# Optimization experiments

Measured on AMD Instinct MI355X. Metric: run time of the kernel, lower is better.

The kernel has to match this reference:

```python
import jax, jax.numpy as jnp
import numpy as np


def _freq_downsample(x, sf):
    # torch: stack(chunk(dim=2), 4) -> cat(chunk(dim=3), 4) -> mean(-1) -> repeat(1,1,sf,sf)
    # equivalent: mean over the sf x sf grid of contiguous blocks, then tile back.
    B, C, H, W = x.shape
    m = x.reshape(B, C, sf, H // sf, sf, W // sf).mean(axis=(2, 4))
    return jnp.tile(m, (1, 1, sf, sf))


def setup_inputs() -> dict:
    key = jax.random.key(0)
    k1, k2, k3 = jax.random.split(key, 3)
    shape = (4, 3, 256, 256)
    return {
        "STy": jax.random.normal(k1, shape, dtype=jnp.float32),
        "Fk_real": jax.random.normal(k2, shape, dtype=jnp.float32),
        "Fk_imag": jax.random.normal(k3, shape, dtype=jnp.float32),
        "sf": 2,
    }


def _forward(STy, Fk_real, Fk_imag, sf, num_iters=50, alpha=1e-6, gam=0.1):
    fft2 = lambda a: jnp.fft.fft2(a, axes=(-2, -1))
    ifft2 = lambda a: jnp.fft.ifft2(a, axes=(-2, -1))

    Fk = jax.lax.complex(Fk_real, Fk_imag)          # complex64 OTF
    FkC = jnp.conj(Fk)
    Fk2 = Fk_real ** 2 + Fk_imag ** 2               # |Fk|^2, real

    FSTy = fft2(STy)
    Fr = FkC * FSTy / (_freq_downsample(Fk2, sf) + alpha)
    pred = ifft2(Fr).real

    # finite-difference stencils DH = [1,-1] horizontal, DV vertical
    DH = jnp.zeros_like(pred).at[..., 0, 0].set(1.0).at[..., 0, 1].set(-1.0)
    DV = jnp.zeros_like(pred).at[..., 0, 0].set(1.0).at[..., 1, 0].set(-1.0)
    FDH, FDV = fft2(DH), fft2(DV)
    FDHC, FDVC = jnp.conj(FDH), jnp.conj(FDV)
    FD2 = jnp.abs(FDV) ** 2 + jnp.abs(FDH) ** 2 + 1e-8  # real

    # loop-invariant terms (identical math to recomputing each iteration)
    den = _freq_downsample(Fk2 / FD2, sf) + alpha
    FkFSTy = FkC * FSTy

    def body(carry, k):
        pred, x_old, t_old, U1, U2, D1, D2 = carry
        gam_k = gam * jnp.exp2(-k / num_iters)      # gam * 0.5 ** (k/num_iters)
        Fr = FkFSTy + alpha * (FDHC * fft2(U1 - D1) + FDVC * fft2(U2 - D2))
        Fr = (Fr - FkC * _freq_downsample(Fk * Fr / FD2, sf) / den) / (alpha * FD2)
        x_new = ifft2(Fr).real
        t_new = (1.0 + jnp.sqrt(1.0 + 4.0 * t_old ** 2)) / 2.0
        pred = x_new + (t_old - 1.0) / t_new * (x_new - x_old)
        DHr = ifft2(Fr * FDH).real
        DVr = ifft2(Fr * FDV).real
        NU1, NU2 = DHr + D1, DVr + D2
        NU = jnp.sqrt(NU1 ** 2 + NU2 ** 2 + 1e-8)
        A = jnp.maximum(0.0, NU - gam_k) + 1e-8
        A = A / (A + gam_k)                         # soft-threshold magnitude shrink
        U1n, U2n = A * NU1, A * NU2
        return (pred, x_new, t_new, U1n, U2n, D1 + DHr - U1n, D2 + DVr - U2n), None

    carry0 = (pred, pred, jnp.float32(1.0), pred, pred,
              jnp.zeros_like(pred), jnp.zeros_like(pred))
    ks = jnp.arange(num_iters, dtype=jnp.float32)
    (pred, *_), _ = jax.lax.scan(body, carry0, ks)
    return pred


def reference(STy, Fk_real, Fk_imag, sf):
    return _forward(STy, Fk_real, Fk_imag, sf)
```

## Files before the change

kernel.cpp:

```cpp
#include <hip/hip_runtime.h>
#include <math.h>

#define NIMG 12
#define NSZ 256
#define HWSZ 65536
#define NBLK 768

__device__ __forceinline__ size_t widx(int n, int u, int j)
{
  int tile = (j & 127) >> 1;
  int slot = (j & 1) + ((j >> 7) << 1);
  return ((((size_t)n << 6) + tile) << 10) + ((size_t)u << 2) + slot;
}

__device__ __forceinline__ void isync(unsigned* flags, int base, int sr, unsigned gen)
{
  __syncthreads();
  int t = threadIdx.x;
  if (t < 64) {
    if (t == 0) {
      __builtin_amdgcn_fence(__ATOMIC_RELEASE, "agent");
      __hip_atomic_store(&flags[base + sr], gen, __ATOMIC_RELAXED, __HIP_MEMORY_SCOPE_AGENT);
    }
    unsigned v;
    do {
      v = __hip_atomic_load(&flags[base + t], __ATOMIC_RELAXED, __HIP_MEMORY_SCOPE_AGENT);
    } while (__any(v < gen));
    __builtin_amdgcn_fence(__ATOMIC_ACQUIRE, "agent");
  }
  __syncthreads();
}

__device__ __forceinline__ void fft256g(float2* A, float2* B, const float2* tw, int lane,
                                        float dir, bool active)
{
  float2* src = A;
  float2* dst = B;
  int m = 1;
#pragma unroll
  for (int s = 0; s < 8; ++s) {
    __syncthreads();
    if (active) {
#pragma unroll
      for (int h = 0; h < 2; ++h) {
        int b = lane + (h << 6);
        int k = b & (m - 1);
        int jm = b - k;
        float2 a = src[b];
        float2 c = src[b + 128];
        float2 w = tw[jm];
        float wr = w.x, wi = dir * w.y;
        float ex = a.x - c.x, ey = a.y - c.y;
        dst[2 * jm + k]     = make_float2(a.x + c.x, a.y + c.y);
        dst[2 * jm + k + m] = make_float2(ex * wr - ey * wi, ex * wi + ey * wr);
      }
    }
    float2* t = src; src = dst; dst = t;
    m <<= 1;
  }
  __syncthreads();
}
__device__ __forceinline__ void fft256(float2* A, float2* B, const float2* tw, int lane, float dir)
{
  fft256g(A, B, tw, lane, dir, true);
}

__device__ __forceinline__ void make_tw(float2* tw, int t)
{
  float s, c;
  sincospif((float)t * (1.0f / 128.0f), &s, &c);
  tw[t] = make_float2(c, s);
}

__device__ __forceinline__ double fdval(const float2* tw, int k)
{
  return 2.0 - 2.0 * (double)tw[k].x;
}

__global__ __launch_bounds__(256, 3) void k_mega(const float* __restrict__ sty,
                                                 const float* __restrict__ fkr,
                                                 const float* __restrict__ fki,
                                                 float2* __restrict__ WG,
                                                 float2* __restrict__ WF,
                                                 float* __restrict__ Dh,
                                                 float* __restrict__ x49,
                                                 float* __restrict__ out,
                                                 float cmom, unsigned* flags)
{
  __shared__ float2 tw[256];
  __shared__ float2 bufA[6][256];
  __shared__ float2 scrB[6][256];
  __shared__ float2 fkL[4][256];
  __shared__ float2 kfL[4][256];
  __shared__ float  dnL[256];
  __shared__ float  D1L[4][256];
  __shared__ float  D2L[4][256];

  float*   aL   = (float*)scrB;
  float*   bL   = ((float*)scrB) + 5 * 256;
  double2* Ml   = (double2*)scrB;
  float*   dsAp = (float*)scrB;

  int t = threadIdx.x;
  make_tw(tw, t);
  int slot = ((blockIdx.x & 7) * 96) + (blockIdx.x >> 3);
  int n = slot >> 6;
  int sr = slot & 63;
  int fbase = n << 6;
  int r0 = sr << 2;
  int j0 = sr << 1;
  int w = t >> 6, lane = t & 63;
  const float sc = 1.0f / 65536.0f;
  size_t cb = ((((size_t)n << 6) + sr) << 10);
  unsigned gen = 0;

  {
    const float* src = sty + (size_t)n * HWSZ + (size_t)(r0 + w) * NSZ;
#pragma unroll
    for (int q = 0; q < 4; ++q) { int j = lane + (q << 6); bufA[w][j] = make_float2(src[j], 0.f); }
    fft256(bufA[w], scrB[w], tw, lane, -1.f);
#pragma unroll
    for (int q = 0; q < 4; ++q) { int j = lane + (q << 6); WG[widx(n, r0 + w, j)] = bufA[w][j]; }
#pragma unroll
    for (int c = 0; c < 4; ++c) {
      int gc = j0 + (c & 1) + ((c >> 1) << 7);
      size_t idx = (size_t)n * HWSZ + (size_t)t * NSZ + gc;
      fkL[c][t] = make_float2(fkr[idx], fki[idx]);
    }
  }
  isync(flags, fbase, sr, ++gen);

  {
#pragma unroll
    for (int q = 0; q < 4; ++q) { int u = lane + (q << 6); bufA[w][u] = WG[cb + (u << 2) + w]; }
    fft256(bufA[w], scrB[w], tw, lane, -1.f);
#pragma unroll
    for (int c = 0; c < 4; ++c) {
      float2 K = fkL[c][t];
      float2 f = bufA[c][t];
      kfL[c][t] = make_float2(K.x * f.x + K.y * f.y, K.x * f.y - K.y * f.x);
    }
    __syncthreads();
    {
      int u0 = t & 127, p = t >> 7;
      double s1 = 0.0, s2 = 0.0;
#pragma unroll
      for (int s = 0; s < 4; ++s) {
        int u = u0 + ((s & 1) << 7);
        int c = p + ((s >> 1) << 1);
        int gc = j0 + (c & 1) + ((c >> 1) << 7);
        double kr = fkL[c][u].x, ki = fkL[c][u].y;
        double k2 = kr * kr + ki * ki;
        double fd2 = fdval(tw, u) + fdval(tw, gc) + 1e-8;
        s1 += k2;
        s2 += k2 / fd2;
      }
      dnL[u0 * 2 + p] = (float)(s2 * 0.25 + 1e-6);
      dsAp[p * 128 + u0] = (float)(s1 * 0.25 + 1e-6);
    }
    __syncthreads();
#pragma unroll
    for (int c = 0; c < 4; ++c) {
      float d = dsAp[(c & 1) * 128 + (t & 127)];
      float2 kf = kfL[c][t];
      bufA[c][t] = make_float2(kf.x / d, kf.y / d);
    }
    fft256(bufA[w], scrB[w], tw, lane, +1.f);
#pragma unroll
    for (int q = 0; q < 4; ++q) { int u = lane + (q << 6); WF[cb + (u << 2) + w] = bufA[w][u]; }
  }
  isync(flags, fbase, sr, ++gen);

  for (int k = 0; k < 50; ++k) {
    float gamp = (k >= 1) ? (float)(0.1 * exp2(-(double)(k - 1) / 50.0)) : 0.f;

    {
      int gr = (r0 + w - 1) & 255;
#pragma unroll
      for (int q = 0; q < 4; ++q) { int j = lane + (q << 6); bufA[w][j] = WF[widx(n, gr, j)]; }
      fft256(bufA[w], scrB[w], tw, lane, +1.f);
    }
    {
      bool act = (w < 2);
      int e = 4 + (w & 1);
      int gr = (r0 + e - 1) & 255;
      if (act) {
#pragma unroll
        for (int q = 0; q < 4; ++q) { int j = lane + (q << 6); bufA[e][j] = WF[widx(n, gr, j)]; }
      }
      fft256g(bufA[e], scrB[e], tw, lane, +1.f, act);
    }
    {
      int jm1 = (t - 1) & 255;
      size_t hR = (((size_t)n << 6) + ((sr + 1) & 63)) << 9;
      size_t hW = (((size_t)n << 6) + sr) << 9;
      const float* DhP = Dh + (size_t)((k + 1) & 1) * (NBLK * 512);
      float* DhW = Dh + (size_t)(k & 1) * (NBLK * 512);
      for (int e = 1; e <= 5; ++e) {
        int gr = (r0 + e - 1) & 255;
        float xc = bufA[e][t].x * sc;
        if (k == 49 && e <= 4) x49[(size_t)n * HWSZ + (size_t)gr * NSZ + t] = xc;
        float a, b;
        if (k == 0) {
          a = xc; b = xc;
          if (e <= 4) { D1L[e - 1][t] = 0.f; D2L[e - 1][t] = 0.f; }
        } else {
          float dhr = xc - bufA[e][jm1].x * sc;
          float dvr = xc - bufA[e - 1][t].x * sc;
          float d1, d2;
          if (e <= 4) { d1 = D1L[e - 1][t]; d2 = D2L[e - 1][t]; }
          else        { d1 = DhP[hR + t];   d2 = DhP[hR + 256 + t]; }
          float nu1 = dhr + d1, nu2 = dvr + d2;
          float nu = sqrtf(nu1 * nu1 + nu2 * nu2 + 1e-8f);
          float A = fmaxf(0.f, nu - gamp) + 1e-8f;
          A = A / (A + gamp);
          float u1 = A * nu1, u2 = A * nu2;
          float d1v = d1 + dhr - u1;
          float d2v = d2 + dvr - u2;
          if (e <= 4) { D1L[e - 1][t] = d1v; D2L[e - 1][t] = d2v; }
          if (e == 1) { DhW[hW + t] = d1v; DhW[hW + 256 + t] = d2v; }
          a = u1 - d1v; b = u2 - d2v;
        }
        aL[(e - 1) * 256 + t] = a;
        bL[(e - 1) * 256 + t] = b;
      }
    }
    __syncthreads();
    {
#pragma unroll
      for (int q = 0; q < 4; ++q) {
        int j = lane + (q << 6);
        int jp1 = (j + 1) & 255;
        float g = aL[w * 256 + j] - aL[w * 256 + jp1] + bL[w * 256 + j] - bL[(w + 1) * 256 + j];
        bufA[w][j] = make_float2(g, 0.f);
      }
      fft256(bufA[w], scrB[w], tw, lane, -1.f);
#pragma unroll
      for (int q = 0; q < 4; ++q) { int j = lane + (q << 6); WG[widx(n, r0 + w, j)] = bufA[w][j]; }
    }
    isync(flags, fbase, sr, ++gen);

    {
#pragma unroll
      for (int q = 0; q < 4; ++q) { int u = lane + (q << 6); bufA[w][u] = WG[cb + (u << 2) + w]; }
      fft256(bufA[w], scrB[w], tw, lane, -1.f);
#pragma unroll
      for (int c = 0; c < 4; ++c) {
        float2 kf = kfL[c][t];
        float2 fg = bufA[c][t];
        bufA[c][t] = make_float2(kf.x + 1e-6f * fg.x, kf.y + 1e-6f * fg.y);
      }
      __syncthreads();
      {
        int u0 = t & 127, p = t >> 7;
        double sx = 0.0, sy = 0.0;
#pragma unroll
        for (int s = 0; s < 4; ++s) {
          int u = u0 + ((s & 1) << 7);
          int c = p + ((s >> 1) << 1);
          int gc = j0 + (c & 1) + ((c >> 1) << 7);
          float2 f1 = bufA[c][u];
          double kr = fkL[c][u].x, ki = fkL[c][u].y;
          double fd2 = fdval(tw, u) + fdval(tw, gc) + 1e-8;
          sx += (kr * (double)f1.x - ki * (double)f1.y) / fd2;
          sy += (kr * (double)f1.y + ki * (double)f1.x) / fd2;
        }
        Ml[p * 128 + u0] = make_double2(sx * 0.25, sy * 0.25);
      }
      __syncthreads();
#pragma unroll
      for (int c = 0; c < 4; ++c) {
        int u = t;
        int gc = j0 + (c & 1) + ((c >> 1) << 7);
        float2 f1 = bufA[c][u];
        double2 m = Ml[(c & 1) * 128 + (u & 127)];
        double den = (double)dnL[(u & 127) * 2 + (c & 1)];
        double kr = fkL[c][u].x, ki = fkL[c][u].y;
        double px = (kr * m.x + ki * m.y) / den;
        double py = (kr * m.y - ki * m.x) / den;
        double fd2 = fdval(tw, u) + fdval(tw, gc) + 1e-8;
        double s2 = 1.0 / (1e-6 * fd2);
        bufA[c][u] = make_float2((float)(((double)f1.x - px) * s2),
                                 (float)(((double)f1.y - py) * s2));
      }
      fft256(bufA[w], scrB[w], tw, lane, +1.f);
#pragma unroll
      for (int q = 0; q < 4; ++q) { int u = lane + (q << 6); WF[cb + (u << 2) + w] = bufA[w][u]; }
    }
    isync(flags, fbase, sr, ++gen);
  }

  {
    int gr = r0 + w;
#pragma unroll
    for (int q = 0; q < 4; ++q) { int j = lane + (q << 6); bufA[w][j] = WF[widx(n, gr, j)]; }
    fft256(bufA[w], scrB[w], tw, lane, +1.f);
    size_t base = (size_t)n * HWSZ + (size_t)gr * NSZ;
#pragma unroll
    for (int q = 0; q < 4; ++q) {
      int j = lane + (q << 6);
      float v = bufA[w][j].x * sc;
      out[base + j] = v + cmom * (v - x49[base + j]);
    }
  }
}

__global__ __launch_bounds__(256) void k_rowfwd_sty(const float* __restrict__ sty,
                                                    float2* __restrict__ Wb)
{
  __shared__ float2 tw[256];
  __shared__ float2 bufA[4][256];
  __shared__ float2 bufB[4][256];
  int t = threadIdx.x;
  make_tw(tw, t);
  int n = blockIdx.x >> 6;
  int r0 = (blockIdx.x & 63) << 2;
  int w = t >> 6, lane = t & 63;
  const float* src = sty + (size_t)n * HWSZ + (size_t)(r0 + w) * NSZ;
#pragma unroll
  for (int q = 0; q < 4; ++q) { int j = lane + (q << 6); bufA[w][j] = make_float2(src[j], 0.f); }
  fft256(bufA[w], bufB[w], tw, lane, -1.f);
  float2* dst = Wb + (size_t)n * HWSZ + (size_t)(r0 + w) * NSZ;
#pragma unroll
  for (int q = 0; q < 4; ++q) { int j = lane + (q << 6); dst[j] = bufA[w][j]; }
}

__global__ __launch_bounds__(256) void k_colsetup(float2* __restrict__ Wb,
                                                  float2* __restrict__ FkF,
                                                  const float* __restrict__ fkr,
                                                  const float* __restrict__ fki,
                                                  float* __restrict__ denq)
{
  __shared__ float2 tw[256];
  __shared__ float2 bufA[4][256];
  __shared__ float2 bufB[4][256];
  __shared__ float dsA[2][128];
  int t = threadIdx.x;
  make_tw(tw, t);
  int n = blockIdx.x >> 6;
  int j0 = (blockIdx.x & 63) << 1;
  int w = t >> 6, lane = t & 63;
  int gcw = j0 + (w & 1) + ((w >> 1) << 7);
  float2* Wn = Wb + (size_t)n * HWSZ;
#pragma unroll
  for (int q = 0; q < 4; ++q) { int u = lane + (q << 6); bufA[w][u] = Wn[(size_t)u * NSZ + gcw]; }
  fft256(bufA[w], bufB[w], tw, lane, -1.f);
#pragma unroll
  for (int c = 0; c < 4; ++c) {
    int u = t;
    int gc = j0 + (c & 1) + ((c >> 1) << 7);
    size_t idx = (size_t)n * HWSZ + (size_t)u * NSZ + gc;
    float kr = fkr[idx], ki = fki[idx];
    float2 f = bufA[c][u];
    float2 kf = make_float2(kr * f.x + ki * f.y, kr * f.y - ki * f.x);
    FkF[idx] = kf;
    bufA[c][u] = kf;
  }
  __syncthreads();
  {
    int u0 = t & 127, p = t >> 7;
    double s1 = 0.0, s2 = 0.0;
#pragma unroll
    for (int s = 0; s < 4; ++s) {
      int u = u0 + ((s & 1) << 7);
      int c = p + ((s >> 1) << 1);
      int gc = j0 + (c & 1) + ((c >> 1) << 7);
      size_t idx = (size_t)n * HWSZ + (size_t)u * NSZ + gc;
      double kr = fkr[idx], ki = fki[idx];
      double k2 = kr * kr + ki * ki;
      double fd2 = fdval(tw, u) + fdval(tw, gc) + 1e-8;
      s1 += k2;
      s2 += k2 / fd2;
    }
    denq[(size_t)n * 16384 + (size_t)u0 * 128 + (j0 + p)] = (float)(s2 * 0.25 + 1e-6);
    dsA[p][u0] = (float)(s1 * 0.25 + 1e-6);
  }
  __syncthreads();
#pragma unroll
  for (int c = 0; c < 4; ++c) {
    int u = t;
    float d = dsA[c & 1][u & 127];
    float2 kf = bufA[c][u];
    bufA[c][u] = make_float2(kf.x / d, kf.y / d);
  }
  fft256(bufA[w], bufB[w], tw, lane, +1.f);
#pragma unroll
  for (int q = 0; q < 4; ++q) { int u = lane + (q << 6); Wn[(size_t)u * NSZ + gcw] = bufA[w][u]; }
}

__global__ __launch_bounds__(256) void k_spatial_rowfwd(const float* __restrict__ x,
                                                        const float* __restrict__ D1p,
                                                        const float* __restrict__ D2p,
                                                        float* __restrict__ D1n,
                                                        float* __restrict__ D2n,
                                                        float2* __restrict__ Wb,
                                                        float gamp, int firstIter)
{
  __shared__ float2 tw[256];
  __shared__ float aL[5][256];
  __shared__ float bL[5][256];
  __shared__ float2 bufA[4][256];
  __shared__ float2 bufB[4][256];
  int t = threadIdx.x;
  make_tw(tw, t);
  int n = blockIdx.x >> 6;
  int r0 = (blockIdx.x & 63) << 2;
  const float* xn = x + (size_t)n * HWSZ;
  for (int rr = 0; rr < 5; ++rr) {
    int i = (r0 + rr) & 255;
    int im1 = (i - 1) & 255;
    int j = t;
    int jm1 = (j - 1) & 255;
    float xc = xn[(size_t)i * NSZ + j];
    float a, b;
    if (firstIter) {
      a = xc; b = xc;
    } else {
      float dhr = xc - xn[(size_t)i * NSZ + jm1];
      float dvr = xc - xn[(size_t)im1 * NSZ + j];
      size_t idx = (size_t)n * HWSZ + (size_t)i * NSZ + j;
      float d1 = D1p[idx], d2 = D2p[idx];
      float nu1 = dhr + d1, nu2 = dvr + d2;
      float nu = sqrtf(nu1 * nu1 + nu2 * nu2 + 1e-8f);
      float A = fmaxf(0.f, nu - gamp) + 1e-8f;
      A = A / (A + gamp);
      float u1 = A * nu1, u2 = A * nu2;
      float d1v = d1 + dhr - u1;
      float d2v = d2 + dvr - u2;
      if (rr < 4) { D1n[idx] = d1v; D2n[idx] = d2v; }
      a = u1 - d1v; b = u2 - d2v;
    }
    aL[rr][j] = a;
    bL[rr][j] = b;
  }
  __syncthreads();
  int w = t >> 6, lane = t & 63;
#pragma unroll
  for (int q = 0; q < 4; ++q) {
    int j = lane + (q << 6);
    int jp1 = (j + 1) & 255;
    float g = aL[w][j] - aL[w][jp1] + bL[w][j] - bL[w + 1][j];
    bufA[w][j] = make_float2(g, 0.f);
  }
  fft256(bufA[w], bufB[w], tw, lane, -1.f);
  float2* dst = Wb + (size_t)n * HWSZ + (size_t)(r0 + w) * NSZ;
#pragma unroll
  for (int q = 0; q < 4; ++q) { int j = lane + (q << 6); dst[j] = bufA[w][j]; }
}

__global__ __launch_bounds__(256) void k_colphase(float2* __restrict__ Wb,
                                                  const float2* __restrict__ FkF,
                                                  const float* __restrict__ fkr,
                                                  const float* __restrict__ fki,
                                                  const float* __restrict__ denq)
{
  __shared__ float2 tw[256];
  __shared__ float2 bufA[4][256];
  __shared__ float2 bufB[4][256];
  __shared__ double2 Ml[2][128];
  int t = threadIdx.x;
  make_tw(tw, t);
  int n = blockIdx.x >> 6;
  int j0 = (blockIdx.x & 63) << 1;
  int w = t >> 6, lane = t & 63;
  int gcw = j0 + (w & 1) + ((w >> 1) << 7);
  float2* Wn = Wb + (size_t)n * HWSZ;
#pragma unroll
  for (int q = 0; q < 4; ++q) { int u = lane + (q << 6); bufA[w][u] = Wn[(size_t)u * NSZ + gcw]; }
  fft256(bufA[w], bufB[w], tw, lane, -1.f);
#pragma unroll
  for (int c = 0; c < 4; ++c) {
    int u = t;
    int gc = j0 + (c & 1) + ((c >> 1) << 7);
    size_t idx = (size_t)n * HWSZ + (size_t)u * NSZ + gc;
    float2 kf = FkF[idx];
    float2 fg = bufA[c][u];
    bufA[c][u] = make_float2(kf.x + 1e-6f * fg.x, kf.y + 1e-6f * fg.y);
  }
  __syncthreads();
  {
    int u0 = t & 127, p = t >> 7;
    double sx = 0.0, sy = 0.0;
#pragma unroll
    for (int s = 0; s < 4; ++s) {
      int u = u0 + ((s & 1) << 7);
      int c = p + ((s >> 1) << 1);
      int gc = j0 + (c & 1) + ((c >> 1) << 7);
      size_t idx = (size_t)n * HWSZ + (size_t)u * NSZ + gc;
      float2 f1 = bufA[c][u];
      double kr = fkr[idx], ki = fki[idx];
      double fd2 = fdval(tw, u) + fdval(tw, gc) + 1e-8;
      sx += (kr * (double)f1.x - ki * (double)f1.y) / fd2;
      sy += (kr * (double)f1.y + ki * (double)f1.x) / fd2;
    }
    Ml[p][u0] = make_double2(sx * 0.25, sy * 0.25);
  }
  __syncthreads();
#pragma unroll
  for (int c = 0; c < 4; ++c) {
    int u = t;
    int gc = j0 + (c & 1) + ((c >> 1) << 7);
    size_t idx = (size_t)n * HWSZ + (size_t)u * NSZ + gc;
    float2 f1 = bufA[c][u];
    double2 m = Ml[c & 1][u & 127];
    double den = (double)denq[(size_t)n * 16384 + (size_t)(u & 127) * 128 + (j0 + (c & 1))];
    double kr = fkr[idx], ki = fki[idx];
    double px = (kr * m.x + ki * m.y) / den;
    double py = (kr * m.y - ki * m.x) / den;
    double fd2 = fdval(tw, u) + fdval(tw, gc) + 1e-8;
    double s2 = 1.0 / (1e-6 * fd2);
    bufA[c][u] = make_float2((float)(((double)f1.x - px) * s2),
                             (float)(((double)f1.y - py) * s2));
  }
  fft256(bufA[w], bufB[w], tw, lane, +1.f);
#pragma unroll
  for (int q = 0; q < 4; ++q) { int u = lane + (q << 6); Wn[(size_t)u * NSZ + gcw] = bufA[w][u]; }
}

__global__ __launch_bounds__(256) void k_rowinv(const float2* __restrict__ Wb,
                                                float* __restrict__ xout,
                                                const float* __restrict__ xold,
                                                float* __restrict__ pred,
                                                float cmom, int isLast)
{
  __shared__ float2 tw[256];
  __shared__ float2 bufA[4][256];
  __shared__ float2 bufB[4][256];
  int t = threadIdx.x;
  make_tw(tw, t);
  int n = blockIdx.x >> 6;
  int r0 = (blockIdx.x & 63) << 2;
  int w = t >> 6, lane = t & 63;
  const float2* src = Wb + (size_t)n * HWSZ + (size_t)(r0 + w) * NSZ;
#pragma unroll
  for (int q = 0; q < 4; ++q) { int j = lane + (q << 6); bufA[w][j] = src[j]; }
  fft256(bufA[w], bufB[w], tw, lane, +1.f);
  size_t base = (size_t)n * HWSZ + (size_t)(r0 + w) * NSZ;
#pragma unroll
  for (int q = 0; q < 4; ++q) {
    int j = lane + (q << 6);
    float v = bufA[w][j].x * (1.0f / 65536.0f);
    xout[base + j] = v;
    if (isLast) pred[base + j] = v + cmom * (v - xold[base + j]);
  }
}

extern "C" void kernel_launch(void* const* d_in, const int* in_sizes, int n_in,
                              void* d_out, int out_size, void* d_ws, size_t ws_size,
                              hipStream_t stream)
{
  (void)in_sizes; (void)n_in; (void)out_size; (void)ws_size;
  const float* STy = (const float*)d_in[0];
  const float* fkr = (const float*)d_in[1];
  const float* fki = (const float*)d_in[2];
  float* out = (float*)d_out;

  char* p = (char*)d_ws;
  const size_t cplx = (size_t)NIMG * HWSZ * sizeof(float2);
  const size_t realb = (size_t)NIMG * HWSZ * sizeof(float);
  float2* WG  = (float2*)p; p += cplx;
  float2* WF  = (float2*)p; p += cplx;
  float2* FkF = (float2*)p; p += cplx;
  float* denq = (float*)p;  p += (size_t)NIMG * 16384 * sizeof(float);
  float* D1a = (float*)p;   p += realb;
  float* D2a = (float*)p;   p += realb;
  float* D1b = (float*)p;   p += realb;
  float* D2b = (float*)p;   p += realb;
  float* xA  = (float*)p;   p += realb;
  float* xB  = (float*)p;   p += realb;
  float* Dh  = (float*)p;   p += (size_t)2 * NBLK * 512 * sizeof(float);
  unsigned* flags = (unsigned*)p; p += 4096;

  double t_old = 1.0, cm = 0.0;
  for (int k = 0; k < 50; ++k) {
    double t_new = (1.0 + sqrt(1.0 + 4.0 * t_old * t_old)) * 0.5;
    if (k == 49) cm = (t_old - 1.0) / t_new;
    t_old = t_new;
  }

  int maxb = 0;
  hipError_t oe = hipOccupancyMaxActiveBlocksPerMultiprocessor(&maxb, k_mega, 256, 0);
  bool coop = (oe == hipSuccess && maxb >= 3);

  dim3 grid(NBLK), blk(256);
  if (coop) {
    hipMemsetAsync(Dh, 0, (size_t)2 * NBLK * 512 * sizeof(float), stream);
    hipMemsetAsync(flags, 0, 4096, stream);
    k_mega<<<grid, blk, 0, stream>>>(STy, fkr, fki, WG, WF, Dh, xA, out, (float)cm, flags);
  } else {
    hipMemsetAsync(D1a, 0, 2 * realb, stream);
    float2* Wb = WG;
    float* x0 = xA; float* x1 = xB;
    k_rowfwd_sty<<<grid, blk, 0, stream>>>(STy, Wb);
    k_colsetup<<<grid, blk, 0, stream>>>(Wb, FkF, fkr, fki, denq);
    k_rowinv<<<grid, blk, 0, stream>>>(Wb, x0, x0, out, 0.f, 0);
    double to = 1.0;
    for (int k = 0; k < 50; ++k) {
      float gamp = (k >= 1) ? (float)(0.1 * exp2(-(double)(k - 1) / 50.0)) : 0.f;
      const float* xk = (k & 1) ? x1 : x0;
      float* xn = (k & 1) ? x0 : x1;
      const float* D1p = (k & 1) ? D1a : D1b;
      const float* D2p = (k & 1) ? D2a : D2b;
      float* D1w = (k & 1) ? D1b : D1a;
      float* D2w = (k & 1) ? D2b : D2a;
      k_spatial_rowfwd<<<grid, blk, 0, stream>>>(xk, D1p, D2p, D1w, D2w, Wb, gamp, (k == 0) ? 1 : 0);
      k_colphase<<<grid, blk, 0, stream>>>(Wb, FkF, fkr, fki, denq);
      double tn = (1.0 + sqrt(1.0 + 4.0 * to * to)) * 0.5;
      int isLast = (k == 49) ? 1 : 0;
      float cmom = (float)((to - 1.0) / tn);
      k_rowinv<<<grid, blk, 0, stream>>>(Wb, xn, xk, out, isLast ? cmom : 0.f, isLast);
      to = tn;
    }
  }
}
```

Measured before the change: 2.498 ms.

## Use wave-local radix-4 FFT with register twiddles and precomputed reciprocals

Replaces the radix-2, 8-stage shared-memory FFT in the persistent mega kernel with a 4-stage radix-4 FFT. Each wavefront transforms its own row, so the per-stage block barriers go away, and twiddles are held in registers instead of a shared table. Loop-invariant frequency-domain denominators (fd2 and den) are computed once per thread as double reciprocals, which turns the per-iteration divisions into multiplies. The spin-wait barrier also gains s_sleep backoff to reduce flag polling pressure. In exchange the wave-local FFT depends on implicit wavefront lockstep for its LDS ordering, and the change raises register pressure.

```diff
diff --git a/kernel.cpp b/kernel.cpp
--- a/kernel.cpp
+++ b/kernel.cpp
@@ -23,7 +23,9 @@
       __hip_atomic_store(&flags[base + sr], gen, __ATOMIC_RELAXED, __HIP_MEMORY_SCOPE_AGENT);
     }
     unsigned v;
+    int it = 0;
     do {
+      if (it++ > 2) __builtin_amdgcn_s_sleep(4);
       v = __hip_atomic_load(&flags[base + t], __ATOMIC_RELAXED, __HIP_MEMORY_SCOPE_AGENT);
     } while (__any(v < gen));
     __builtin_amdgcn_fence(__ATOMIC_ACQUIRE, "agent");
@@ -31,50 +33,49 @@
   __syncthreads();
 }
 
-__device__ __forceinline__ void fft256g(float2* A, float2* B, const float2* tw, int lane,
-                                        float dir, bool active)
-{
-  float2* src = A;
-  float2* dst = B;
-  int m = 1;
-#pragma unroll
-  for (int s = 0; s < 8; ++s) {
-    __syncthreads();
-    if (active) {
-#pragma unroll
-      for (int h = 0; h < 2; ++h) {
-        int b = lane + (h << 6);
-        int k = b & (m - 1);
-        int jm = b - k;
-        float2 a = src[b];
-        float2 c = src[b + 128];
-        float2 w = tw[jm];
-        float wr = w.x, wi = dir * w.y;
-        float ex = a.x - c.x, ey = a.y - c.y;
-        dst[2 * jm + k]     = make_float2(a.x + c.x, a.y + c.y);
-        dst[2 * jm + k + m] = make_float2(ex * wr - ey * wi, ex * wi + ey * wr);
-      }
-    }
-    float2* t = src; src = dst; dst = t;
-    m <<= 1;
-  }
-  __syncthreads();
-}
-__device__ __forceinline__ void fft256(float2* A, float2* B, const float2* tw, int lane, float dir)
-{
-  fft256g(A, B, tw, lane, dir, true);
-}
-
-__device__ __forceinline__ void make_tw(float2* tw, int t)
+__device__ __forceinline__ void r4_bfly(const float2* __restrict__ S, float2* __restrict__ D,
+                                        int b, int m, float2 w1, float2 w2, float2 w3,
+                                        float dir, bool usetw)
+{
+  int k = b & (m - 1);
+  int base = ((b - k) << 2) + k;
+  float2 x0 = S[b], x1 = S[b + 64], x2 = S[b + 128], x3 = S[b + 192];
+  float t0x = x0.x + x2.x, t0y = x0.y + x2.y;
+  float t1x = x0.x - x2.x, t1y = x0.y - x2.y;
+  float t2x = x1.x + x3.x, t2y = x1.y + x3.y;
+  float e3x = x1.x - x3.x, e3y = x1.y - x3.y;
+  float t3x = -dir * e3y, t3y = dir * e3x;
+  D[base] = make_float2(t0x + t2x, t0y + t2y);
+  float y1x = t1x + t3x, y1y = t1y + t3y;
+  float y2x = t0x - t2x, y2y = t0y - t2y;
+  float y3x = t1x - t3x, y3y = t1y - t3y;
+  if (usetw) {
+    float w1i = dir * w1.y, w2i = dir * w2.y, w3i = dir * w3.y;
+    D[base + m]     = make_float2(y1x * w1.x - y1y * w1i, y1x * w1i + y1y * w1.x);
+    D[base + 2 * m] = make_float2(y2x * w2.x - y2y * w2i, y2x * w2i + y2y * w2.x);
+    D[base + 3 * m] = make_float2(y3x * w3.x - y3y * w3i, y3x * w3i + y3y * w3.x);
+  } else {
+    D[base + m]     = make_float2(y1x, y1y);
+    D[base + 2 * m] = make_float2(y2x, y2y);
+    D[base + 3 * m] = make_float2(y3x, y3y);
+  }
+}
+
+struct Tw { float2 a1, a2, a3, b1, b2, b3, c1, c2, c3; };
+
+__device__ __forceinline__ float2 mktw(int q)
 {
   float s, c;
-  sincospif((float)t * (1.0f / 128.0f), &s, &c);
-  tw[t] = make_float2(c, s);
-}
-
-__device__ __forceinline__ double fdval(const float2* tw, int k)
-{
-  return 2.0 - 2.0 * (double)tw[k].x;
+  sincospif((float)q * (1.0f / 128.0f), &s, &c);
+  return make_float2(c, s);
+}
+
+__device__ __forceinline__ void fft4_row(float2* A, float2* B, int lane, float dir, const Tw& tw)
+{
+  r4_bfly(A, B, lane, 1,  tw.a1, tw.a2, tw.a3, dir, true);
+  r4_bfly(B, A, lane, 4,  tw.b1, tw.b2, tw.b3, dir, true);
+  r4_bfly(A, B, lane, 16, tw.c1, tw.c2, tw.c3, dir, true);
+  r4_bfly(B, A, lane, 64, tw.a1, tw.a1, tw.a1, dir, false);
 }
 
 __global__ __launch_bounds__(256, 3) void k_mega(const float* __restrict__ sty,
@@ -87,9 +88,8 @@
                                                  float* __restrict__ out,
                                                  float cmom, unsigned* flags)
 {
-  __shared__ float2 tw[256];
-  __shared__ float2 bufA[6][256];
-  __shared__ float2 scrB[6][256];
+  __shared__ __align__(16) float2 bufA[6][256];
+  __shared__ __align__(16) float2 scrB[6][256];
   __shared__ float2 fkL[4][256];
   __shared__ float2 kfL[4][256];
   __shared__ float  dnL[256];
@@ -102,7 +102,6 @@
   float*   dsAp = (float*)scrB;
 
   int t = threadIdx.x;
-  make_tw(tw, t);
   int slot = ((blockIdx.x & 7) * 96) + (blockIdx.x >> 3);
   int n = slot >> 6;
   int sr = slot & 63;
@@ -114,11 +113,41 @@
   size_t cb = ((((size_t)n << 6) + sr) << 10);
   unsigned gen = 0;
 
+  Tw tw;
+  {
+    int qa = lane, qb = lane & ~3, qc = lane & ~15;
+    tw.a1 = mktw(qa);  tw.a2 = mktw(2 * qa); tw.a3 = mktw(3 * qa);
+    tw.b1 = mktw(qb);  tw.b2 = mktw(2 * qb); tw.b3 = mktw(3 * qb);
+    tw.c1 = mktw(qc);  tw.c2 = mktw(2 * qc); tw.c3 = mktw(3 * qc);
+  }
+  int u0 = t & 127, pp = t >> 7;
+  double fdgc[4], rM[4], rF[4];
+  double rdn0, rdn1;
+  {
+    double s;
+    s = sinpi((double)u0 * (1.0 / 256.0));        double fdu0 = 4.0 * s * s;
+    s = sinpi((double)(u0 + 128) * (1.0 / 256.0)); double fdu1 = 4.0 * s * s;
+#pragma unroll
+    for (int c = 0; c < 4; ++c) {
+      int gc = j0 + (c & 1) + ((c >> 1) << 7);
+      s = sinpi((double)gc * (1.0 / 256.0));
+      fdgc[c] = 4.0 * s * s;
+    }
+#pragma unroll
+    for (int s4 = 0; s4 < 4; ++s4) {
+      double fdu = (s4 & 1) ? fdu1 : fdu0;
+      rM[s4] = 1.0 / (fdu + fdgc[pp + ((s4 >> 1) << 1)] + 1e-8);
+    }
+    double fdt = pp ? fdu1 : fdu0;
+#pragma unroll
+    for (int c = 0; c < 4; ++c) rF[c] = 1.0 / (fdt + fdgc[c] + 1e-8);
+  }
+
   {
     const float* src = sty + (size_t)n * HWSZ + (size_t)(r0 + w) * NSZ;
 #pragma unroll
     for (int q = 0; q < 4; ++q) { int j = lane + (q << 6); bufA[w][j] = make_float2(src[j], 0.f); }
-    fft256(bufA[w], scrB[w], tw, lane, -1.f);
+    fft4_row(bufA[w], scrB[w], lane, -1.f, tw);
 #pragma unroll
     for (int q = 0; q < 4; ++q) { int j = lane + (q << 6); WG[widx(n, r0 + w, j)] = bufA[w][j]; }
 #pragma unroll
@@ -133,39 +162,39 @@
   {
 #pragma unroll
     for (int q = 0; q < 4; ++q) { int u = lane + (q << 6); bufA[w][u] = WG[cb + (u << 2) + w]; }
-    fft256(bufA[w], scrB[w], tw, lane, -1.f);
+    fft4_row(bufA[w], scrB[w], lane, -1.f, tw);
+    __syncthreads();
 #pragma unroll
     for (int c = 0; c < 4; ++c) {
       float2 K = fkL[c][t];
       float2 f = bufA[c][t];
       kfL[c][t] = make_float2(K.x * f.x + K.y * f.y, K.x * f.y - K.y * f.x);
     }
-    __syncthreads();
     {
-      int u0 = t & 127, p = t >> 7;
       double s1 = 0.0, s2 = 0.0;
 #pragma unroll
-      for (int s = 0; s < 4; ++s) {
-        int u = u0 + ((s & 1) << 7);
-        int c = p + ((s >> 1) << 1);
-        int gc = j0 + (c & 1) + ((c >> 1) << 7);
+      for (int s4 = 0; s4 < 4; ++s4) {
+        int u = u0 + ((s4 & 1) << 7);
+        int c = pp + ((s4 >> 1) << 1);
         double kr = fkL[c][u].x, ki = fkL[c][u].y;
         double k2 = kr * kr + ki * ki;
-        double fd2 = fdval(tw, u) + fdval(tw, gc) + 1e-8;
         s1 += k2;
-        s2 += k2 / fd2;
-      }
-      dnL[u0 * 2 + p] = (float)(s2 * 0.25 + 1e-6);
-      dsAp[p * 128 + u0] = (float)(s1 * 0.25 + 1e-6);
+        s2 += k2 * rM[s4];
+      }
+      dnL[u0 * 2 + pp] = (float)(s2 * 0.25 + 1e-6);
+      dsAp[pp * 128 + u0] = (float)(s1 * 0.25 + 1e-6);
     }
     __syncthreads();
+    rdn0 = 1.0 / (double)dnL[u0 * 2];
+    rdn1 = 1.0 / (double)dnL[u0 * 2 + 1];
 #pragma unroll
     for (int c = 0; c < 4; ++c) {
-      float d = dsAp[(c & 1) * 128 + (t & 127)];
+      float d = dsAp[(c & 1) * 128 + u0];
       float2 kf = kfL[c][t];
       bufA[c][t] = make_float2(kf.x / d, kf.y / d);
     }
-    fft256(bufA[w], scrB[w], tw, lane, +1.f);
+    __syncthreads();
+    fft4_row(bufA[w], scrB[w], lane, +1.f, tw);
 #pragma unroll
     for (int q = 0; q < 4; ++q) { int u = lane + (q << 6); WF[cb + (u << 2) + w] = bufA[w][u]; }
   }
@@ -178,18 +207,16 @@
       int gr = (r0 + w - 1) & 255;
 #pragma unroll
       for (int q = 0; q < 4; ++q) { int j = lane + (q << 6); bufA[w][j] = WF[widx(n, gr, j)]; }
-      fft256(bufA[w], scrB[w], tw, lane, +1.f);
-    }
-    {
-      bool act = (w < 2);
-      int e = 4 + (w & 1);
-      int gr = (r0 + e - 1) & 255;
-      if (act) {
-#pragma unroll
-        for (int q = 0; q < 4; ++q) { int j = lane + (q << 6); bufA[e][j] = WF[widx(n, gr, j)]; }
-      }
-      fft256g(bufA[e], scrB[e], tw, lane, +1.f, act);
-    }
+      fft4_row(bufA[w], scrB[w], lane, +1.f, tw);
+      if (w < 2) {
+        int e = 4 + w;
+        int gr2 = (r0 + e - 1) & 255;
+#pragma unroll
+        for (int q = 0; q < 4; ++q) { int j = lane + (q << 6); bufA[e][j] = WF[widx(n, gr2, j)]; }
+        fft4_row(bufA[e], scrB[e], lane, +1.f, tw);
+      }
+    }
+    __syncthreads();
     {
       int jm1 = (t - 1) & 255;
       size_t hR = (((size_t)n << 6) + ((sr + 1) & 63)) << 9;
@@ -234,7 +261,7 @@
         float g = aL[w * 256 + j] - aL[w * 256 + jp1] + bL[w * 256 + j] - bL[(w + 1) * 256 + j];
         bufA[w][j] = make_float2(g, 0.f);
       }
-      fft256(bufA[w], scrB[w], tw, lane, -1.f);
+      fft4_row(bufA[w], scrB[w], lane, -1.f, tw);
 #pragma unroll
       for (int q = 0; q < 4; ++q) { int j = lane + (q << 6); WG[widx(n, r0 + w, j)] = bufA[w][j]; }
     }
@@ -243,7 +270,8 @@
     {
 #pragma unroll
       for (int q = 0; q < 4; ++q) { int u = lane + (q << 6); bufA[w][u] = WG[cb + (u << 2) + w]; }
-      fft256(bufA[w], scrB[w], tw, lane, -1.f);
+      fft4_row(bufA[w], scrB[w], lane, -1.f, tw);
+      __syncthreads();
 #pragma unroll
       for (int c = 0; c < 4; ++c) {
         float2 kf = kfL[c][t];
@@ -252,38 +280,33 @@
       }
       __syncthreads();
       {
-        int u0 = t & 127, p = t >> 7;
         double sx = 0.0, sy = 0.0;
 #pragma unroll
-        for (int s = 0; s < 4; ++s) {
-          int u = u0 + ((s & 1) << 7);
-          int c = p + ((s >> 1) << 1);
-          int gc = j0 + (c & 1) + ((c >> 1) << 7);
+        for (int s4 = 0; s4 < 4; ++s4) {
+          int u = u0 + ((s4 & 1) << 7);
+          int c = pp + ((s4 >> 1) << 1);
           float2 f1 = bufA[c][u];
           double kr = fkL[c][u].x, ki = fkL[c][u].y;
-          double fd2 = fdval(tw, u) + fdval(tw, gc) + 1e-8;
-          sx += (kr * (double)f1.x - ki * (double)f1.y) / fd2;
-          sy += (kr * (double)f1.y + ki * (double)f1.x) / fd2;
+          sx += (kr * (double)f1.x - ki * (double)f1.y) * rM[s4];
+          sy += (kr * (double)f1.y + ki * (double)f1.x) * rM[s4];
         }
-        Ml[p * 128 + u0] = make_double2(sx * 0.25, sy * 0.25);
+        Ml[pp * 128 + u0] = make_double2(sx * 0.25, sy * 0.25);
       }
       __syncthreads();
 #pragma unroll
       for (int c = 0; c < 4; ++c) {
-        int u = t;
-        int gc = j0 + (c & 1) + ((c >> 1) << 7);
-        float2 f1 = bufA[c][u];
-        double2 m = Ml[(c & 1) * 128 + (u & 127)];
-        double den = (double)dnL[(u & 127) * 2 + (c & 1)];
-        double kr = fkL[c][u].x, ki = fkL[c][u].y;
-        double px = (kr * m.x + ki * m.y) / den;
-        double py = (kr * m.y - ki * m.x) / den;
-        double fd2 = fdval(tw, u) + fdval(tw, gc) + 1e-8;
-        double s2 = 1.0 / (1e-6 * fd2);
-        bufA[c][u] = make_float2((float)(((double)f1.x - px) * s2),
+        float2 f1 = bufA[c][t];
+        double2 m = Ml[(c & 1) * 128 + u0];
+        double rden = (c & 1) ? rdn1 : rdn0;
+        double kr = fkL[c][t].x, ki = fkL[c][t].y;
+        double px = (kr * m.x + ki * m.y) * rden;
+        double py = (kr * m.y - ki * m.x) * rden;
+        double s2 = 1e6 * rF[c];
+        bufA[c][t] = make_float2((float)(((double)f1.x - px) * s2),
                                  (float)(((double)f1.y - py) * s2));
       }
-      fft256(bufA[w], scrB[w], tw, lane, +1.f);
+      __syncthreads();
+      fft4_row(bufA[w], scrB[w], lane, +1.f, tw);
 #pragma unroll
       for (int q = 0; q < 4; ++q) { int u = lane + (q << 6); WF[cb + (u << 2) + w] = bufA[w][u]; }
     }
@@ -294,7 +317,7 @@
     int gr = r0 + w;
 #pragma unroll
     for (int q = 0; q < 4; ++q) { int j = lane + (q << 6); bufA[w][j] = WF[widx(n, gr, j)]; }
-    fft256(bufA[w], scrB[w], tw, lane, +1.f);
+    fft4_row(bufA[w], scrB[w], lane, +1.f, tw);
     size_t base = (size_t)n * HWSZ + (size_t)gr * NSZ;
 #pragma unroll
     for (int q = 0; q < 4; ++q) {
@@ -305,21 +328,65 @@
   }
 }
 
+__device__ __forceinline__ void fft256g(float2* A, float2* B, const float2* twl, int lane,
+                                        float dir, bool active)
+{
+  float2* src = A;
+  float2* dst = B;
+  int m = 1;
+#pragma unroll
+  for (int s = 0; s < 8; ++s) {
+    __syncthreads();
+    if (active) {
+#pragma unroll
+      for (int h = 0; h < 2; ++h) {
+        int b = lane + (h << 6);
+        int k = b & (m - 1);
+        int jm = b - k;
+        float2 a = src[b];
+        float2 c = src[b + 128];
+        float2 wv = twl[jm];
+        float wr = wv.x, wi = dir * wv.y;
+        float ex = a.x - c.x, ey = a.y - c.y;
+        dst[2 * jm + k]     = make_float2(a.x + c.x, a.y + c.y);
+        dst[2 * jm + k + m] = make_float2(ex * wr - ey * wi, ex * wi + ey * wr);
+      }
+    }
+    float2* t = src; src = dst; dst = t;
+    m <<= 1;
+  }
+  __syncthreads();
+}
+__device__ __forceinline__ void fft256(float2* A, float2* B, const float2* twl, int lane, float dir)
+{
+  fft256g(A, B, twl, lane, dir, true);
+}
+__device__ __forceinline__ void make_tw(float2* twl, int t)
+{
+  float s, c;
+  sincospif((float)t * (1.0f / 128.0f), &s, &c);
+  twl[t] = make_float2(c, s);
+}
+__device__ __forceinline__ double fdval(const float2* twl, int k)
+{
+  return 2.0 - 2.0 * (double)twl[k].x;
+}
+
 __global__ __launch_bounds__(256) void k_rowfwd_sty(const float* __restrict__ sty,
                                                     float2* __restrict__ Wb)
 {
-  __shared__ float2 tw[256];
+  __shared__ float2 twl[256];
   __shared__ float2 bufA[4][256];
   __shared__ float2 bufB[4][256];
   int t = threadIdx.x;
-  make_tw(tw, t);
+  make_tw(twl, t);
   int n = blockIdx.x >> 6;
   int r0 = (blockIdx.x & 63) << 2;
   int w = t >> 6, lane = t & 63;
   const float* src = sty + (size_t)n * HWSZ + (size_t)(r0 + w) * NSZ;
 #pragma unroll
   for (int q = 0; q < 4; ++q) { int j = lane + (q << 6); bufA[w][j] = make_float2(src[j], 0.f); }
-  fft256(bufA[w], bufB[w], tw, lane, -1.f);
+  fft256(bufA[w], bufB[w], twl, lane, -1.f);
   float2* dst = Wb + (size_t)n * HWSZ + (size_t)(r0 + w) * NSZ;
 #pragma unroll
   for (int q = 0; q < 4; ++q) { int j = lane + (q << 6); dst[j] = bufA[w][j]; }
@@ -331,12 +398,12 @@
                                                   const float* __restrict__ fki,
                                                   float* __restrict__ denq)
 {
-  __shared__ float2 tw[256];
+  __shared__ float2 twl[256];
   __shared__ float2 bufA[4][256];
   __shared__ float2 bufB[4][256];
   __shared__ float dsA[2][128];
   int t = threadIdx.x;
-  make_tw(tw, t);
+  make_tw(twl, t);
   int n = blockIdx.x >> 6;
   int j0 = (blockIdx.x & 63) << 1;
   int w = t >> 6, lane = t & 63;
@@ -344,7 +411,7 @@
   float2* Wn = Wb + (size_t)n * HWSZ;
 #pragma unroll
   for (int q = 0; q < 4; ++q) { int u = lane + (q << 6); bufA[w][u] = Wn[(size_t)u * NSZ + gcw]; }
-  fft256(bufA[w], bufB[w], tw, lane, -1.f);
+  fft256(bufA[w], bufB[w], twl, lane, -1.f);
 #pragma unroll
   for (int c = 0; c < 4; ++c) {
     int u = t;
@@ -368,7 +435,7 @@
       size_t idx = (size_t)n * HWSZ + (size_t)u * NSZ + gc;
       double kr = fkr[idx], ki = fki[idx];
       double k2 = kr * kr + ki * ki;
-      double fd2 = fdval(tw, u) + fdval(tw, gc) + 1e-8;
+      double fd2 = fdval(twl, u) + fdval(twl, gc) + 1e-8;
       s1 += k2;
       s2 += k2 / fd2;
     }
@@ -383,7 +450,7 @@
     float2 kf = bufA[c][u];
     bufA[c][u] = make_float2(kf.x / d, kf.y / d);
   }
-  fft256(bufA[w], bufB[w], tw, lane, +1.f);
+  fft256(bufA[w], bufB[w], twl, lane, +1.f);
 #pragma unroll
   for (int q = 0; q < 4; ++q) { int u = lane + (q << 6); Wn[(size_t)u * NSZ + gcw] = bufA[w][u]; }
 }
@@ -396,13 +463,13 @@
                                                         float2* __restrict__ Wb,
                                                         float gamp, int firstIter)
 {
-  __shared__ float2 tw[256];
+  __shared__ float2 twl[256];
   __shared__ float aL[5][256];
   __shared__ float bL[5][256];
   __shared__ float2 bufA[4][256];
   __shared__ float2 bufB[4][256];
   int t = threadIdx.x;
-  make_tw(tw, t);
+  make_tw(twl, t);
   int n = blockIdx.x >> 6;
   int r0 = (blockIdx.x & 63) << 2;
   const float* xn = x + (size_t)n * HWSZ;
@@ -442,7 +509,7 @@
     float g = aL[w][j] - aL[w][jp1] + bL[w][j] - bL[w + 1][j];
     bufA[w][j] = make_float2(g, 0.f);
   }
-  fft256(bufA[w], bufB[w], tw, lane, -1.f);
+  fft256(bufA[w], bufB[w], twl, lane, -1.f);
   float2* dst = Wb + (size_t)n * HWSZ + (size_t)(r0 + w) * NSZ;
 #pragma unroll
   for (int q = 0; q < 4; ++q) { int j = lane + (q << 6); dst[j] = bufA[w][j]; }
@@ -454,12 +521,12 @@
                                                   const float* __restrict__ fki,
                                                   const float* __restrict__ denq)
 {
-  __shared__ float2 tw[256];
+  __shared__ float2 twl[256];
   __shared__ float2 bufA[4][256];
   __shared__ float2 bufB[4][256];
-  __shared__ double2 Ml[2][128];
+  __shared__ double2 Mll[2][128];
   int t = threadIdx.x;
-  make_tw(tw, t);
+  make_tw(twl, t);
   int n = blockIdx.x >> 6;
   int j0 = (blockIdx.x & 63) << 1;
   int w = t >> 6, lane = t & 63;
@@ -467,7 +534,7 @@
   float2* Wn = Wb + (size_t)n * HWSZ;
 #pragma unroll
   for (int q = 0; q < 4; ++q) { int u = lane + (q << 6); bufA[w][u] = Wn[(size_t)u * NSZ + gcw]; }
-  fft256(bufA[w], bufB[w], tw, lane, -1.f);
+  fft256(bufA[w], bufB[w], twl, lane, -1.f);
 #pragma unroll
   for (int c = 0; c < 4; ++c) {
     int u = t;
@@ -489,11 +556,11 @@
       size_t idx = (size_t)n * HWSZ + (size_t)u * NSZ + gc;
       float2 f1 = bufA[c][u];
       double kr = fkr[idx], ki = fki[idx];
-      double fd2 = fdval(tw, u) + fdval(tw, gc) + 1e-8;
+      double fd2 = fdval(twl, u) + fdval(twl, gc) + 1e-8;
       sx += (kr * (double)f1.x - ki * (double)f1.y) / fd2;
       sy += (kr * (double)f1.y + ki * (double)f1.x) / fd2;
     }
-    Ml[p][u0] = make_double2(sx * 0.25, sy * 0.25);
+    Mll[p][u0] = make_double2(sx * 0.25, sy * 0.25);
   }
   __syncthreads();
 #pragma unroll
@@ -502,17 +569,17 @@
     int gc = j0 + (c & 1) + ((c >> 1) << 7);
     size_t idx = (size_t)n * HWSZ + (size_t)u * NSZ + gc;
     float2 f1 = bufA[c][u];
-    double2 m = Ml[c & 1][u & 127];
+    double2 m = Mll[c & 1][u & 127];
     double den = (double)denq[(size_t)n * 16384 + (size_t)(u & 127) * 128 + (j0 + (c & 1))];
     double kr = fkr[idx], ki = fki[idx];
     double px = (kr * m.x + ki * m.y) / den;
     double py = (kr * m.y - ki * m.x) / den;
-    double fd2 = fdval(tw, u) + fdval(tw, gc) + 1e-8;
+    double fd2 = fdval(twl, u) + fdval(twl, gc) + 1e-8;
     double s2 = 1.0 / (1e-6 * fd2);
     bufA[c][u] = make_float2((float)(((double)f1.x - px) * s2),
                              (float)(((double)f1.y - py) * s2));
   }
-  fft256(bufA[w], bufB[w], tw, lane, +1.f);
+  fft256(bufA[w], bufB[w], twl, lane, +1.f);
 #pragma unroll
   for (int q = 0; q < 4; ++q) { int u = lane + (q << 6); Wn[(size_t)u * NSZ + gcw] = bufA[w][u]; }
 }
@@ -523,18 +590,18 @@
                                                 float* __restrict__ pred,
                                                 float cmom, int isLast)
 {
-  __shared__ float2 tw[256];
+  __shared__ float2 twl[256];
   __shared__ float2 bufA[4][256];
   __shared__ float2 bufB[4][256];
   int t = threadIdx.x;
-  make_tw(tw, t);
+  make_tw(twl, t);
   int n = blockIdx.x >> 6;
   int r0 = (blockIdx.x & 63) << 2;
   int w = t >> 6, lane = t & 63;
   const float2* src = Wb + (size_t)n * HWSZ + (size_t)(r0 + w) * NSZ;
 #pragma unroll
   for (int q = 0; q < 4; ++q) { int j = lane + (q << 6); bufA[w][j] = src[j]; }
-  fft256(bufA[w], bufB[w], tw, lane, +1.f);
+  fft256(bufA[w], bufB[w], twl, lane, +1.f);
   size_t base = (size_t)n * HWSZ + (size_t)(r0 + w) * NSZ;
 #pragma unroll
   for (int q = 0; q < 4; ++q) {
```

Result: no change. 2.485 ms (-0.5%).
